# Kernel optimization log

Hardware: AMD Instinct MI355X
Metric: run time of the kernel (lower is better)

## Reference

```python
import jax, jax.numpy as jnp
import numpy as np

C = 256
CQK = C // 8


def setup_inputs() -> dict:
    key = jax.random.key(0)
    ks = jax.random.split(key, 8)
    B, H, W = 4, 64, 64
    inputs = jax.random.normal(ks[0], (B, H, W, C), dtype=jnp.float32)
    s = 1.0 / np.sqrt(C)
    Wq = jax.random.normal(ks[1], (C, CQK), dtype=jnp.float32) * s
    bq = jnp.zeros((CQK,), dtype=jnp.float32)
    Wk = jax.random.normal(ks[2], (C, CQK), dtype=jnp.float32) * s
    bk = jnp.zeros((CQK,), dtype=jnp.float32)
    Wv = jax.random.normal(ks[3], (C, C), dtype=jnp.float32) * s
    bv = jnp.zeros((C,), dtype=jnp.float32)
    gamma = jnp.float32(0.7)  # nonzero so attention branch contributes
    return {"inputs": inputs, "Wq": Wq, "bq": bq, "Wk": Wk, "bk": bk,
            "Wv": Wv, "bv": bv, "gamma": gamma}


def reference(inputs, Wq, bq, Wk, bk, Wv, bv, gamma):
    B, H, W, Cin = inputs.shape
    N = H * W
    x = inputs.reshape(B, N, Cin)
    # 1x1 convs == per-pixel channel matmuls
    q = x @ Wq + bq                      # (B, N, C//8)
    k = x @ Wk + bk                      # (B, N, C//8)
    v = x @ Wv + bv                      # (B, N, C)
    energy = jnp.einsum('bnd,bmd->bnm', q, k)   # (B, N, N), no scale (faithful)
    attn = jax.nn.softmax(energy, axis=-1)
    x_out = jnp.einsum('bnm,bmc->bnc', attn, v)  # (B, N, C)
    out = gamma * x_out.reshape(B, H, W, Cin) + inputs
    return out
```

## Files before the change

### kernel.cpp

```cpp
#include <hip/hip_runtime.h>
#include <hip/hip_bf16.h>

#define B_ 4
#define N_ 4096
#define C_ 256
#define D_ 32
#define LOG2E 1.44269504088896340736f
#define MFMA16 __builtin_amdgcn_mfma_f32_16x16x32_bf16

typedef __attribute__((ext_vector_type(8))) short short8;
typedef __attribute__((ext_vector_type(4))) short short4v;
typedef __attribute__((ext_vector_type(4))) float float4v;

__device__ inline short f2bf_rne(float f) {
  unsigned u = __builtin_bit_cast(unsigned, f);
  u += 0x7FFFu + ((u >> 16) & 1u);
  return (short)(u >> 16);
}
__device__ inline float bf2f(short s) {
  unsigned u = ((unsigned)(unsigned short)s) << 16;
  return __builtin_bit_cast(float, u);
}
__device__ inline float fast_exp2(float x) { return __builtin_amdgcn_exp2f(x); }

__device__ inline short4v pk4_bf16(float p0, float p1, float p2, float p3) {
  union { unsigned u[2]; short4v s; } r;
  asm("v_cvt_pk_bf16_f32 %0, %1, %2" : "=v"(r.u[0]) : "v"(p0), "v"(p1));
  asm("v_cvt_pk_bf16_f32 %0, %1, %2" : "=v"(r.u[1]) : "v"(p2), "v"(p3));
  return r.s;
}

__global__ __launch_bounds__(256) void cast_w_kernel(
    const float* __restrict__ Wq, const float* __restrict__ Wk,
    const float* __restrict__ Wv, short* __restrict__ WtF) {
  int i  = blockIdx.x * 256 + threadIdx.x;
  int j  = i & 7;
  int l  = (i >> 3) & 63;
  int ks = (i >> 9) & 7;
  int nb = i >> 12;
  int n  = nb * 16 + (l & 15);
  int k  = ks * 32 + ((l >> 4) << 3) + j;
  float v;
  if (n < 32)      v = Wq[k * 32 + n] * LOG2E;
  else if (n < 64) v = Wk[k * 32 + (n - 32)];
  else             v = Wv[k * 256 + (n - 64)];
  WtF[i] = f2bf_rne(v);
}

__global__ __launch_bounds__(256, 2) void proj_kernel(
    const float* __restrict__ x, const short* __restrict__ WtF,
    const float* __restrict__ bq, const float* __restrict__ bk,
    const float* __restrict__ bv,
    short* __restrict__ qb, short* __restrict__ kF, short* __restrict__ vF) {
  int blk = blockIdx.x;
  int b  = blk >> 7;
  int r0 = (blk & 127) * 32;
  int t  = threadIdx.x;
  int w  = t >> 6;
  int l  = t & 63;
  int lc = l & 15;
  int q4 = l >> 4;

  __shared__ __align__(16) short sA[32][272];
  __shared__ __align__(16) short sV[256][40];
  __shared__ __align__(16) short sK[32][36];

  {
    const float* xb = x + (size_t)(b * N_ + r0) * C_;
#pragma unroll
    for (int ch = 0; ch < 8; ch++) {
      int f   = ch * 256 + t;
      int row = f >> 6;
      int col = (f & 63) * 4;
      float4v v = *(const float4v*)(xb + f * 4);
      short4v s = pk4_bf16(v[0], v[1], v[2], v[3]);
      *(short4v*)(&sA[row][col]) = s;
    }
  }
  __syncthreads();

  float4v acc[10];
#pragma unroll
  for (int i = 0; i < 10; i++) { acc[i][0] = 0.f; acc[i][1] = 0.f; acc[i][2] = 0.f; acc[i][3] = 0.f; }

  const short* wbase = WtF + w * 4096 + l * 8;

#define LOADW(B0, B1, B2, B3, B4, KS)                       \
  B0 = *(const short8*)(wbase + (KS) * 512 + 0 * 16384);    \
  B1 = *(const short8*)(wbase + (KS) * 512 + 1 * 16384);    \
  B2 = *(const short8*)(wbase + (KS) * 512 + 2 * 16384);    \
  B3 = *(const short8*)(wbase + (KS) * 512 + 3 * 16384);    \
  B4 = *(const short8*)(wbase + (KS) * 512 + 4 * 16384);

#define DO_MFMA(A0, A1, B0, B1, B2, B3, B4)                 \
  acc[0] = MFMA16(A0, B0, acc[0], 0, 0, 0);                 \
  acc[1] = MFMA16(A1, B0, acc[1], 0, 0, 0);                 \
  acc[2] = MFMA16(A0, B1, acc[2], 0, 0, 0);                 \
  acc[3] = MFMA16(A1, B1, acc[3], 0, 0, 0);                 \
  acc[4] = MFMA16(A0, B2, acc[4], 0, 0, 0);                 \
  acc[5] = MFMA16(A1, B2, acc[5], 0, 0, 0);                 \
  acc[6] = MFMA16(A0, B3, acc[6], 0, 0, 0);                 \
  acc[7] = MFMA16(A1, B3, acc[7], 0, 0, 0);                 \
  acc[8] = MFMA16(A0, B4, acc[8], 0, 0, 0);                 \
  acc[9] = MFMA16(A1, B4, acc[9], 0, 0, 0);

  short8 wA0, wA1, wA2, wA3, wA4, wB0, wB1, wB2, wB3, wB4;
  LOADW(wA0, wA1, wA2, wA3, wA4, 0)
#pragma unroll
  for (int kk = 0; kk < 8; kk += 2) {
    short8 a00 = *(const short8*)(&sA[lc][kk * 32 + q4 * 8]);
    short8 a01 = *(const short8*)(&sA[16 + lc][kk * 32 + q4 * 8]);
    LOADW(wB0, wB1, wB2, wB3, wB4, kk + 1)
    DO_MFMA(a00, a01, wA0, wA1, wA2, wA3, wA4)
    short8 a10 = *(const short8*)(&sA[lc][(kk + 1) * 32 + q4 * 8]);
    short8 a11 = *(const short8*)(&sA[16 + lc][(kk + 1) * 32 + q4 * 8]);
    LOADW(wA0, wA1, wA2, wA3, wA4, kk + 2)
    DO_MFMA(a10, a11, wB0, wB1, wB2, wB3, wB4)
  }
#undef LOADW
#undef DO_MFMA

  {
    float bias0 = (w < 2) ? bq[w * 16 + lc] * LOG2E : bk[(w - 2) * 16 + lc];
#pragma unroll
    for (int rt = 0; rt < 2; rt++) {
      if (w < 2) {
#pragma unroll
        for (int r = 0; r < 4; r++) {
          int row = rt * 16 + q4 * 4 + r;
          qb[(size_t)(b * N_ + r0 + row) * D_ + w * 16 + lc] =
              f2bf_rne(acc[rt][r] + bias0);
        }
      } else {
#pragma unroll
        for (int r = 0; r < 4; r++) {
          int row = rt * 16 + q4 * 4 + r;
          sK[row][(w - 2) * 16 + lc] = f2bf_rne(acc[rt][r] + bias0);
        }
      }
    }
#pragma unroll
    for (int nbo = 1; nbo < 5; nbo++) {
      float bias = bv[(nbo - 1) * 64 + w * 16 + lc];
#pragma unroll
      for (int rt = 0; rt < 2; rt++) {
        float4v a = acc[nbo * 2 + rt];
        short4v pk = pk4_bf16(a[0] + bias, a[1] + bias, a[2] + bias, a[3] + bias);
        *(short4v*)(&sV[(nbo - 1) * 64 + w * 16 + lc][rt * 16 + q4 * 4]) = pk;
      }
    }
  }
  __syncthreads();

  int kt  = r0 >> 6;
  int ks0 = (r0 >> 5) & 1;

  {
    size_t tb2 = ((size_t)(b * 64 + kt) * 32 + ks0 * 16) * 512;
    int cb = t >> 4;
#pragma unroll
    for (int k = 0; k < 4; k++) {
      int p = (t & 15) * 4 + k;
      int j = p >> 4, i = p & 15;
      short8 vv = *(const short8*)(&sV[cb * 16 + i][j * 8]);
      *(short8*)(vF + tb2 + (size_t)t * 32 + k * 8) = vv;
    }
  }
  if (t < 128) {
    int fr = t >> 6, ll = t & 63;
    int kv = fr * 16 + (ll & 15), dg = ll >> 4;
    size_t tbk = ((size_t)(b * 64 + kt) * 4 + ks0 * 2) * 512;
    short8 kv8 = *(const short8*)(&sK[kv][dg * 8]);
    *(short8*)(kF + tbk + (size_t)t * 8) = kv8;
  }
}

__global__ __launch_bounds__(512, 4) void flash_partial_kernel(
    const short* __restrict__ qb, const short* __restrict__ kF,
    const short* __restrict__ vF, short* __restrict__ obuf,
    float* __restrict__ lbuf) {
  int blk = blockIdx.x;
  int b  = blk & 3;
  int hb = (blk >> 2) & 1;
  int qt = blk >> 3;
  int r0 = qt * 64;
  int t  = threadIdx.x;
  int w  = t >> 6;
  int l  = t & 63;
  int lc = l & 15;
  int q4 = l >> 4;
  int rq = w & 3;
  int kh = w >> 2;

  __shared__ __align__(16) short sPn[2][4096];
  __shared__ float sL[4][16];

  int p = (b * 64 + qt) * 2 + hb;

  short8 qf = *(const short8*)(qb + (size_t)(b * N_ + r0 + rq * 16 + lc) * D_ + q4 * 8);

  const short* kbp = kF + ((size_t)(b * 64 + hb * 32) * 4) * 512 + kh * 1024 + l * 8;
  const short* vbp = vF + ((size_t)(b * 64 + hb * 32) * 32 + 2 * w) * 512 + l * 8;

  short8 kC0, kC1;
  short8 vX00, vX01, vX10, vX11;
  short8 vY00, vY01, vY10, vY11;

  kC0 = *(const short8*)(kbp + 0);
  kC1 = *(const short8*)(kbp + 512);
  vX00 = *(const short8*)(vbp + 0);
  vX01 = *(const short8*)(vbp + 512);
  vX10 = *(const short8*)(vbp + 8192);
  vX11 = *(const short8*)(vbp + 8704);

  float4v O[8];
#pragma unroll
  for (int i = 0; i < 8; i++) { O[i][0] = 0.f; O[i][1] = 0.f; O[i][2] = 0.f; O[i][3] = 0.f; }
  float l_part = 0.f;

  int qkbase = (rq * 2) * 512 + (((q4 >> 1) * 16) + lc) * 8 + (q4 & 1) * 4;

#define K_RELOAD(TI)                                                           \
  { size_t o_ = (size_t)(TI) * 2048;                                           \
    kC0 = *(const short8*)(kbp + o_);                                          \
    kC1 = *(const short8*)(kbp + o_ + 512); }

#define QK_STEP(SPB, VALID)                                                    \
  { __builtin_amdgcn_s_setprio(1);                                             \
    float4v z; z[0] = 0.f; z[1] = 0.f; z[2] = 0.f; z[3] = 0.f;                 \
    float4v S0 = MFMA16(kC0, qf, z, 0, 0, 0);                                  \
    float4v S1 = MFMA16(kC1, qf, z, 0, 0, 0);                                  \
    short* rowp = &sPn[SPB][qkbase + kh * 512];                                \
    float ts = 0.f;                                                            \
    { float p0 = fast_exp2(S0[0]), p1 = fast_exp2(S0[1]);                      \
      float p2 = fast_exp2(S0[2]), p3 = fast_exp2(S0[3]);                      \
      ts += (p0 + p1) + (p2 + p3);                                             \
      *(short4v*)(rowp + 0) = pk4_bf16(p0, p1, p2, p3); }                      \
    { float p0 = fast_exp2(S1[0]), p1 = fast_exp2(S1[1]);                      \
      float p2 = fast_exp2(S1[2]), p3 = fast_exp2(S1[3]);                      \
      ts += (p0 + p1) + (p2 + p3);                                             \
      *(short4v*)(rowp + 256) = pk4_bf16(p0, p1, p2, p3); }                    \
    __builtin_amdgcn_s_setprio(0);                                             \
    if (VALID) l_part += ts; }

#define PV_STEP(SPB, V00, V01, V10, V11)                                       \
  { _Pragma("unroll")                                                          \
    for (int rt = 0; rt < 4; rt++) {                                           \
      short8 pf0 = *(const short8*)(&sPn[SPB][(rt * 2 + 0) * 512 + l * 8]);    \
      short8 pf1 = *(const short8*)(&sPn[SPB][(rt * 2 + 1) * 512 + l * 8]);    \
      O[rt * 2 + 0] = MFMA16(pf0, V00, O[rt * 2 + 0], 0, 0, 0);                \
      O[rt * 2 + 0] = MFMA16(pf1, V10, O[rt * 2 + 0], 0, 0, 0);                \
      O[rt * 2 + 1] = MFMA16(pf0, V01, O[rt * 2 + 1], 0, 0, 0);                \
      O[rt * 2 + 1] = MFMA16(pf1, V11, O[rt * 2 + 1], 0, 0, 0);                \
    } }

  QK_STEP(0, true)
  K_RELOAD(1)
  __syncthreads();

  for (int ti = 0; ti < 32; ti += 2) {
    int n1 = ti + 1;
    int n2 = (ti + 2 < 32) ? ti + 2 : 31;
    bool v2 = (ti + 2 < 32);
    int n3 = (ti + 3 < 32) ? ti + 3 : 31;

    { size_t vo = (size_t)n1 * 16384;
      vY00 = *(const short8*)(vbp + vo);
      vY01 = *(const short8*)(vbp + vo + 512);
      vY10 = *(const short8*)(vbp + vo + 8192);
      vY11 = *(const short8*)(vbp + vo + 8704); }
    QK_STEP(1, true)
    K_RELOAD(n2)
    PV_STEP(0, vX00, vX01, vX10, vX11)
    __syncthreads();

    { size_t vo = (size_t)n2 * 16384;
      vX00 = *(const short8*)(vbp + vo);
      vX01 = *(const short8*)(vbp + vo + 512);
      vX10 = *(const short8*)(vbp + vo + 8192);
      vX11 = *(const short8*)(vbp + vo + 8704); }
    QK_STEP(0, v2)
    K_RELOAD(n3)
    PV_STEP(1, vY00, vY01, vY10, vY11)
    __syncthreads();
  }
#undef K_RELOAD
#undef QK_STEP
#undef PV_STEP

  {
    short* ob = obuf + ((size_t)p * 64 + w * 8) * 256 + l * 4;
#pragma unroll
    for (int a = 0; a < 8; a++) {
      float4v o = O[a];
      *(short4v*)(ob + a * 256) = pk4_bf16(o[0], o[1], o[2], o[3]);
    }
  }
  {
    float l_tot = l_part + __shfl_xor(l_part, 16, 64);
    l_tot += __shfl_xor(l_tot, 32, 64);
    if (kh == 0 && q4 == 0) sL[rq][lc] = l_tot;
    __syncthreads();
    if (kh == 1 && q4 == 0)
      lbuf[(size_t)p * 64 + rq * 16 + lc] = l_tot + sL[rq][lc];
  }
}

__global__ __launch_bounds__(256) void merge_kernel(
    const short* __restrict__ obuf, const float* __restrict__ lbuf,
    const float* __restrict__ xin, const float* __restrict__ gptr,
    float* __restrict__ out) {
  int blk2 = blockIdx.x;
  int blk  = blk2 >> 1;
  int h    = blk2 & 1;
  int t    = threadIdx.x;
  float g  = *gptr;

  __shared__ float sS[32][260];
  __shared__ float sGLinv[32];

  const short* o0 = obuf + (size_t)(blk * 2 + 0) * 16384;
  const short* o1 = obuf + (size_t)(blk * 2 + 1) * 16384;
  const float* l0 = lbuf + (size_t)(blk * 2 + 0) * 64;
  const float* l1 = lbuf + (size_t)(blk * 2 + 1) * 64;
  size_t gbase = (size_t)blk * 16384;

  if (t < 32)
    sGLinv[t] = g * __builtin_amdgcn_rcpf(l0[32 * h + t] + l1[32 * h + t]);

#pragma unroll
  for (int j = 0; j < 4; j++) {
    int gdx    = j * 256 + t;
    int chunk  = gdx >> 7;
    int within = gdx & 127;
    int offs   = (chunk * 8 + 4 * h) * 256 + within * 8;
    short8 a8 = *(const short8*)(o0 + offs);
    short8 c8 = *(const short8*)(o1 + offs);
    int s_in  = within >> 5;
    int pos8  = within & 31;
    int rt    = 2 * h + (s_in >> 1);
    int cbo   = s_in & 1;
    int chB   = chunk * 32 + cbo * 16;
#pragma unroll
    for (int e = 0; e < 8; e++) {
      int lane = pos8 * 2 + (e >> 2);
      int r    = e & 3;
      int row  = (rt & 1) * 16 + (lane >> 4) * 4 + r;
      int ch   = chB + (lane & 15);
      sS[row][ch] = bf2f(a8[e]) + bf2f(c8[e]);
    }
  }
  __syncthreads();

#pragma unroll
  for (int j = 0; j < 8; j++) {
    int gdx = j * 1024 + t * 4;
    int row = gdx >> 8;
    int ch  = gdx & 255;
    float gl = sGLinv[row];
    size_t gi = gbase + (size_t)(32 * h) * 256 + gdx;
    float4v xv = *(const float4v*)(xin + gi);
    float4v sv = *(const float4v*)(&sS[row][ch]);
    float4v ov;
#pragma unroll
    for (int e = 0; e < 4; e++) ov[e] = sv[e] * gl + xv[e];
    *(float4v*)(out + gi) = ov;
  }
}

extern "C" void kernel_launch(void* const* d_in, const int* in_sizes, int n_in,
                              void* d_out, int out_size, void* d_ws, size_t ws_size,
                              hipStream_t stream) {
  const float* x     = (const float*)d_in[0];
  const float* Wq    = (const float*)d_in[1];
  const float* bq    = (const float*)d_in[2];
  const float* Wk    = (const float*)d_in[3];
  const float* bk    = (const float*)d_in[4];
  const float* Wv    = (const float*)d_in[5];
  const float* bv    = (const float*)d_in[6];
  const float* gamma = (const float*)d_in[7];
  float* out = (float*)d_out;

  char* ws = (char*)d_ws;
  short* qb   = (short*)ws;
  short* kF   = (short*)(ws + (1u << 20));
  short* vF   = (short*)(ws + (2u << 20));
  short* WtF  = (short*)(ws + (10u << 20));
  short* obuf = (short*)(ws + (11u << 20));
  float* lbuf = (float*)(ws + (28u << 20));

  hipLaunchKernelGGL(cast_w_kernel,        dim3(320), dim3(256), 0, stream, Wq, Wk, Wv, WtF);
  hipLaunchKernelGGL(proj_kernel,          dim3(512), dim3(256), 0, stream, x, WtF, bq, bk, bv, qb, kF, vF);
  hipLaunchKernelGGL(flash_partial_kernel, dim3(512), dim3(512), 0, stream, qb, kF, vF, obuf, lbuf);
  hipLaunchKernelGGL(merge_kernel,         dim3(512), dim3(256), 0, stream, obuf, lbuf, x, gamma, out);
}
```

Measured before the change: 140.2 us.

## Keep softmax probabilities in registers via ds_bpermute instead of shared-memory staging

The flash partial kernel no longer writes the exponentiated scores to a double-buffered LDS tile that other waves read back after a barrier. Each wave now computes QK for its own query rows over all keys, repacks the probabilities across lanes with ds_bpermute into the MFMA A-operand layout, and multiplies by its half of the V channels. This removes every __syncthreads and the LDS store/load traffic in the main loop, along with the cross-wave reduction of the row sum. In exchange, each pair of waves recomputes the same QK products and exps, the explicit register prefetch of K and V is dropped, and the output row mapping is changed to match the new split.

```diff
diff --git a/kernel.cpp b/kernel.cpp
--- a/kernel.cpp
+++ b/kernel.cpp
@@ -28,6 +28,11 @@
   asm("v_cvt_pk_bf16_f32 %0, %1, %2" : "=v"(r.u[0]) : "v"(p0), "v"(p1));
   asm("v_cvt_pk_bf16_f32 %0, %1, %2" : "=v"(r.u[1]) : "v"(p2), "v"(p3));
   return r.s;
+}
+__device__ inline unsigned pk2_bf16(float a, float b) {
+  unsigned r;
+  asm("v_cvt_pk_bf16_f32 %0, %1, %2" : "=v"(r) : "v"(a), "v"(b));
+  return r;
 }
 
 __global__ __launch_bounds__(256) void cast_w_kernel(
@@ -190,119 +195,95 @@
   int lc = l & 15;
   int q4 = l >> 4;
   int rq = w & 3;
-  int kh = w >> 2;
-
-  __shared__ __align__(16) short sPn[2][4096];
-  __shared__ float sL[4][16];
+  int cho = w >> 2;
 
   int p = (b * 64 + qt) * 2 + hb;
 
   short8 qf = *(const short8*)(qb + (size_t)(b * N_ + r0 + rq * 16 + lc) * D_ + q4 * 8);
 
-  const short* kbp = kF + ((size_t)(b * 64 + hb * 32) * 4) * 512 + kh * 1024 + l * 8;
-  const short* vbp = vF + ((size_t)(b * 64 + hb * 32) * 32 + 2 * w) * 512 + l * 8;
-
-  short8 kC0, kC1;
-  short8 vX00, vX01, vX10, vX11;
-  short8 vY00, vY01, vY10, vY11;
-
-  kC0 = *(const short8*)(kbp + 0);
-  kC1 = *(const short8*)(kbp + 512);
-  vX00 = *(const short8*)(vbp + 0);
-  vX01 = *(const short8*)(vbp + 512);
-  vX10 = *(const short8*)(vbp + 8192);
-  vX11 = *(const short8*)(vbp + 8704);
+  const short* ktile = kF + ((size_t)(b * 64 + hb * 32) * 4) * 512 + l * 8;
+  const short* vtile = vF + ((size_t)(b * 64 + hb * 32) * 32) * 512
+                          + (size_t)cho * 4096 + l * 8;
+
+  int s1 = (lc + ((q4 & 1) << 5)) * 4;
+  int s2 = s1 + 64;
+  bool ghi = (q4 >= 2);
 
   float4v O[8];
 #pragma unroll
   for (int i = 0; i < 8; i++) { O[i][0] = 0.f; O[i][1] = 0.f; O[i][2] = 0.f; O[i][3] = 0.f; }
   float l_part = 0.f;
 
-  int qkbase = (rq * 2) * 512 + (((q4 >> 1) * 16) + lc) * 8 + (q4 & 1) * 4;
-
-#define K_RELOAD(TI)                                                           \
-  { size_t o_ = (size_t)(TI) * 2048;                                           \
-    kC0 = *(const short8*)(kbp + o_);                                          \
-    kC1 = *(const short8*)(kbp + o_ + 512); }
-
-#define QK_STEP(SPB, VALID)                                                    \
-  { __builtin_amdgcn_s_setprio(1);                                             \
+#define CHUNK(KVH, KC0, KC1)                                                   \
+  { const short* vt_ = vtc + (KVH) * 8192;                                     \
+    short8 v0 = *(const short8*)(vt_ + 0);                                     \
+    short8 v1 = *(const short8*)(vt_ + 512);                                   \
+    short8 v2 = *(const short8*)(vt_ + 1024);                                  \
+    short8 v3 = *(const short8*)(vt_ + 1536);                                  \
+    short8 v4 = *(const short8*)(vt_ + 2048);                                  \
+    short8 v5 = *(const short8*)(vt_ + 2560);                                  \
+    short8 v6 = *(const short8*)(vt_ + 3072);                                  \
+    short8 v7 = *(const short8*)(vt_ + 3584);                                  \
     float4v z; z[0] = 0.f; z[1] = 0.f; z[2] = 0.f; z[3] = 0.f;                 \
-    float4v S0 = MFMA16(kC0, qf, z, 0, 0, 0);                                  \
-    float4v S1 = MFMA16(kC1, qf, z, 0, 0, 0);                                  \
-    short* rowp = &sPn[SPB][qkbase + kh * 512];                                \
-    float ts = 0.f;                                                            \
-    { float p0 = fast_exp2(S0[0]), p1 = fast_exp2(S0[1]);                      \
-      float p2 = fast_exp2(S0[2]), p3 = fast_exp2(S0[3]);                      \
-      ts += (p0 + p1) + (p2 + p3);                                             \
-      *(short4v*)(rowp + 0) = pk4_bf16(p0, p1, p2, p3); }                      \
-    { float p0 = fast_exp2(S1[0]), p1 = fast_exp2(S1[1]);                      \
-      float p2 = fast_exp2(S1[2]), p3 = fast_exp2(S1[3]);                      \
-      ts += (p0 + p1) + (p2 + p3);                                             \
-      *(short4v*)(rowp + 256) = pk4_bf16(p0, p1, p2, p3); }                    \
-    __builtin_amdgcn_s_setprio(0);                                             \
-    if (VALID) l_part += ts; }
-
-#define PV_STEP(SPB, V00, V01, V10, V11)                                       \
-  { _Pragma("unroll")                                                          \
-    for (int rt = 0; rt < 4; rt++) {                                           \
-      short8 pf0 = *(const short8*)(&sPn[SPB][(rt * 2 + 0) * 512 + l * 8]);    \
-      short8 pf1 = *(const short8*)(&sPn[SPB][(rt * 2 + 1) * 512 + l * 8]);    \
-      O[rt * 2 + 0] = MFMA16(pf0, V00, O[rt * 2 + 0], 0, 0, 0);                \
-      O[rt * 2 + 0] = MFMA16(pf1, V10, O[rt * 2 + 0], 0, 0, 0);                \
-      O[rt * 2 + 1] = MFMA16(pf0, V01, O[rt * 2 + 1], 0, 0, 0);                \
-      O[rt * 2 + 1] = MFMA16(pf1, V11, O[rt * 2 + 1], 0, 0, 0);                \
-    } }
-
-  QK_STEP(0, true)
-  K_RELOAD(1)
-  __syncthreads();
-
-  for (int ti = 0; ti < 32; ti += 2) {
-    int n1 = ti + 1;
-    int n2 = (ti + 2 < 32) ? ti + 2 : 31;
-    bool v2 = (ti + 2 < 32);
-    int n3 = (ti + 3 < 32) ? ti + 3 : 31;
-
-    { size_t vo = (size_t)n1 * 16384;
-      vY00 = *(const short8*)(vbp + vo);
-      vY01 = *(const short8*)(vbp + vo + 512);
-      vY10 = *(const short8*)(vbp + vo + 8192);
-      vY11 = *(const short8*)(vbp + vo + 8704); }
-    QK_STEP(1, true)
-    K_RELOAD(n2)
-    PV_STEP(0, vX00, vX01, vX10, vX11)
-    __syncthreads();
-
-    { size_t vo = (size_t)n2 * 16384;
-      vX00 = *(const short8*)(vbp + vo);
-      vX01 = *(const short8*)(vbp + vo + 512);
-      vX10 = *(const short8*)(vbp + vo + 8192);
-      vX11 = *(const short8*)(vbp + vo + 8704); }
-    QK_STEP(0, v2)
-    K_RELOAD(n3)
-    PV_STEP(1, vY00, vY01, vY10, vY11)
-    __syncthreads();
-  }
-#undef K_RELOAD
-#undef QK_STEP
-#undef PV_STEP
-
-  {
-    short* ob = obuf + ((size_t)p * 64 + w * 8) * 256 + l * 4;
-#pragma unroll
-    for (int a = 0; a < 8; a++) {
-      float4v o = O[a];
-      *(short4v*)(ob + a * 256) = pk4_bf16(o[0], o[1], o[2], o[3]);
+    float4v S0 = MFMA16(KC0, qf, z, 0, 0, 0);                                  \
+    float4v S1 = MFMA16(KC1, qf, z, 0, 0, 0);                                  \
+    float e0 = fast_exp2(S0[0]), e1 = fast_exp2(S0[1]);                        \
+    float e2 = fast_exp2(S0[2]), e3 = fast_exp2(S0[3]);                        \
+    float e4 = fast_exp2(S1[0]), e5 = fast_exp2(S1[1]);                        \
+    float e6 = fast_exp2(S1[2]), e7 = fast_exp2(S1[3]);                        \
+    l_part += ((e0 + e1) + (e2 + e3)) + ((e4 + e5) + (e6 + e7));               \
+    unsigned X0 = pk2_bf16(e0, e1), X1 = pk2_bf16(e2, e3);                     \
+    unsigned Y0 = pk2_bf16(e4, e5), Y1 = pk2_bf16(e6, e7);                     \
+    unsigned aX0 = (unsigned)__builtin_amdgcn_ds_bpermute(s1, (int)X0);        \
+    unsigned aX1 = (unsigned)__builtin_amdgcn_ds_bpermute(s1, (int)X1);        \
+    unsigned aY0 = (unsigned)__builtin_amdgcn_ds_bpermute(s1, (int)Y0);        \
+    unsigned aY1 = (unsigned)__builtin_amdgcn_ds_bpermute(s1, (int)Y1);        \
+    unsigned bX0 = (unsigned)__builtin_amdgcn_ds_bpermute(s2, (int)X0);        \
+    unsigned bX1 = (unsigned)__builtin_amdgcn_ds_bpermute(s2, (int)X1);        \
+    unsigned bY0 = (unsigned)__builtin_amdgcn_ds_bpermute(s2, (int)Y0);        \
+    unsigned bY1 = (unsigned)__builtin_amdgcn_ds_bpermute(s2, (int)Y1);        \
+    union { unsigned u[4]; short8 s8; } pa_;                                   \
+    pa_.u[0] = ghi ? aY0 : aX0;                                                \
+    pa_.u[1] = ghi ? aY1 : aX1;                                                \
+    pa_.u[2] = ghi ? bY0 : bX0;                                                \
+    pa_.u[3] = ghi ? bY1 : bX1;                                                \
+    short8 A = pa_.s8;                                                         \
+    O[0] = MFMA16(A, v0, O[0], 0, 0, 0);                                       \
+    O[1] = MFMA16(A, v1, O[1], 0, 0, 0);                                       \
+    O[2] = MFMA16(A, v2, O[2], 0, 0, 0);                                       \
+    O[3] = MFMA16(A, v3, O[3], 0, 0, 0);                                       \
+    O[4] = MFMA16(A, v4, O[4], 0, 0, 0);                                       \
+    O[5] = MFMA16(A, v5, O[5], 0, 0, 0);                                       \
+    O[6] = MFMA16(A, v6, O[6], 0, 0, 0);                                       \
+    O[7] = MFMA16(A, v7, O[7], 0, 0, 0); }
+
+  for (int ti = 0; ti < 32; ++ti) {
+    const short* ktc = ktile + (size_t)ti * 2048;
+    const short* vtc = vtile + (size_t)ti * 16384;
+    short8 k0 = *(const short8*)(ktc + 0);
+    short8 k1 = *(const short8*)(ktc + 512);
+    short8 k2 = *(const short8*)(ktc + 1024);
+    short8 k3 = *(const short8*)(ktc + 1536);
+    CHUNK(0, k0, k1)
+    CHUNK(1, k2, k3)
+  }
+#undef CHUNK
+
+  {
+#pragma unroll
+    for (int cbl = 0; cbl < 8; cbl++) {
+      int gcb = cho * 8 + cbl;
+      int s   = (gcb >> 1) * 8 + rq * 2 + (gcb & 1);
+      float4v o = O[cbl];
+      *(short4v*)(obuf + ((size_t)p * 64 + s) * 256 + l * 4) =
+          pk4_bf16(o[0], o[1], o[2], o[3]);
     }
   }
   {
     float l_tot = l_part + __shfl_xor(l_part, 16, 64);
     l_tot += __shfl_xor(l_tot, 32, 64);
-    if (kh == 0 && q4 == 0) sL[rq][lc] = l_tot;
-    __syncthreads();
-    if (kh == 1 && q4 == 0)
-      lbuf[(size_t)p * 64 + rq * 16 + lc] = l_tot + sL[rq][lc];
+    if (cho == 0 && q4 == 0)
+      lbuf[(size_t)p * 64 + rq * 16 + lc] = l_tot;
   }
 }
 
```

After: 201.2 us. +43.6%, slower.
